# Kernel optimization log

Hardware: AMD Instinct MI355X
Metric: run time of the kernel (lower is better)

## Reference

```python
import jax, jax.numpy as jnp
import numpy as np

# Dimensions (see shape_source)
N = 50000       # graph_size (number of nodes)
E_HALF = 300000 # undirected edges
E = 2 * E_HALF  # directed edges (both orientations)
D = 4           # stalk dimension d
H = 32          # hidden_channels


def _build_graph(seed=0):
    """Symmetric directed edge list: columns [0,E_HALF) are (u->v), columns
    [E_HALF, E) are the reversed (v->u). opp_idx[e] is the index of the
    opposite orientation of edge e (this is exactly the pairing computed by
    lap.compute_left_right_map_index in the torch module)."""
    rng = np.random.default_rng(seed)
    u = rng.integers(0, N, size=E_HALF)
    v = rng.integers(0, N, size=E_HALF)
    v = np.where(v == u, (v + 1) % N, v)  # no self-loops
    edge_index = np.stack([np.concatenate([u, v]), np.concatenate([v, u])]).astype(np.int32)
    opp = np.concatenate([np.arange(E_HALF) + E_HALF, np.arange(E_HALF)]).astype(np.int32)
    return jnp.asarray(edge_index), jnp.asarray(opp)


def setup_inputs() -> dict:
    key = jax.random.key(0)
    k1, k2, k3 = jax.random.split(key, 3)
    edge_index, opp_idx = _build_graph()
    x = jax.random.normal(k1, (N, D, H), dtype=jnp.float32)
    Maps = jax.random.normal(k2, (E, D, D), dtype=jnp.float32)
    # linear1: torch.nn.Linear(d*d, prod(out_shape)) with out_shape=(d,d)
    W1 = jax.random.normal(k3, (D * D, D * D), dtype=jnp.float32) / np.sqrt(D * D)
    b1 = jnp.zeros((D * D,), dtype=jnp.float32)
    return {"x": x, "Maps": Maps, "W1": W1, "b1": b1,
            "edge_index": edge_index, "opp_idx": opp_idx}


def reference(x, Maps, W1, b1, edge_index, opp_idx):
    # The dual-graph (nodes = directed edges) sheaf Laplacian of the
    # GeneralLaplacianBuilder reduces to a closed per-edge block form:
    # every dual node has degree 1, so deg-normalisation (deg_normalised=True,
    # augmented=False) is the identity. For directed edge e = (s -> t) with
    # opposite edge e' = opp_idx[e]:
    #   diag block of dual node e           =  X_s X_s^T
    #   off-diag block between e and e'     = -X_s X_t^T
    # spmm(L, Maps^T-blocks) followed by the x2 and transpose in forward gives
    #   sims_e = 2 * ( M_e (X_s X_s^T) - M_{e'} (X_t X_s^T) )
    s, t = edge_index[0], edge_index[1]
    Xs = x[s]                                   # (E, D, H) gather
    Xt = x[t]                                   # (E, D, H) gather
    G_ss = jnp.einsum('edh,ekh->edk', Xs, Xs)   # (E, D, D)  X_s X_s^T
    G_ts = jnp.einsum('edh,ekh->edk', Xt, Xs)   # (E, D, D)  X_t X_s^T
    sims = 2.0 * (jnp.einsum('eij,ejk->eik', Maps, G_ss)
                  - jnp.einsum('eij,ejk->eik', Maps[opp_idx], G_ts))
    # linear1 (torch Linear: y = x W^T + b) + tanh activation
    flat = sims.reshape(E, D * D) @ W1.T + b1
    return jnp.tanh(flat).reshape(E, D, D)      # out_shape = (d, d)
```

## Files before the change

kernel.cpp:

```cpp
#include <hip/hip_runtime.h>

constexpr int TPB = 256;

__device__ __forceinline__ float fast_tanh(float v) {
    float ex = __expf(2.0f * v);
    return 1.0f - 2.0f * __builtin_amdgcn_rcpf(ex + 1.0f);
}

template <int CTRL>
__device__ __forceinline__ float dppadd(float x) {
    return x + __int_as_float(__builtin_amdgcn_update_dpp(
        0, __float_as_int(x), CTRL, 0xf, 0xf, true));
}
template <int CTRL>
__device__ __forceinline__ float dppmax(float x) {
    return fmaxf(x, __int_as_float(__builtin_amdgcn_update_dpp(
        0, __float_as_int(x), CTRL, 0xf, 0xf, true)));
}

__device__ __forceinline__ float rowsum16(float x) {
    x = dppadd<0x128>(x);
    x = dppadd<0x124>(x);
    x = dppadd<0x122>(x);
    x = dppadd<0x121>(x);
    return x;
}
__device__ __forceinline__ float rowmax16(float x) {
    x = dppmax<0x128>(x);
    x = dppmax<0x124>(x);
    x = dppmax<0x122>(x);
    x = dppmax<0x121>(x);
    return x;
}

__device__ __forceinline__ float2 unpack_q(unsigned int w) {
    return make_float2((float)((int)(w << 16) >> 16), (float)((int)w >> 16));
}

__global__ __launch_bounds__(TPB) void pack_q16_kernel(
    const float* __restrict__ x, uint4* __restrict__ xq,
    float* __restrict__ xscale, int N)
{
    const int tid  = blockIdx.x * TPB + threadIdx.x;
    const int node = tid >> 4, l = tid & 15;
    if (node >= N) return;
    const float* xr = x + (size_t)node * 128 + 2 * l;
    float2 f[4]; float m = 0.f;
    #pragma unroll
    for (int d = 0; d < 4; ++d) {
        f[d] = *(const float2*)(xr + d * 32);
        m = fmaxf(m, fmaxf(fabsf(f[d].x), fabsf(f[d].y)));
    }
    m = rowmax16(m);
    const float inv = m > 0.f ? 32767.0f / m : 0.f;
    unsigned int w[4];
    #pragma unroll
    for (int d = 0; d < 4; ++d) {
        int ix = (int)rintf(f[d].x * inv);
        int iy = (int)rintf(f[d].y * inv);
        w[d] = ((unsigned int)ix & 0xFFFFu) | ((unsigned int)iy << 16);
    }
    xq[(size_t)node * 16 + l] = make_uint4(w[0], w[1], w[2], w[3]);
    if (l == 0) xscale[node] = m * (1.0f / 32767.0f);
}

__global__ __launch_bounds__(TPB) void sheaf_q16_kernel(
    const uint4* __restrict__ xq,
    const float* __restrict__ xscale,
    const float* __restrict__ Maps,
    const float* __restrict__ W1,
    const float* __restrict__ b1,
    const int*   __restrict__ edge_index,
    const int*   __restrict__ opp_idx,
    float*       __restrict__ out,
    int E, int EHALF)
{
    const int tid  = threadIdx.x;
    const int l    = tid & 15;
    const int pair = (blockIdx.x * TPB + tid) >> 4;
    if (pair >= EHALF) return;

    const int s  = edge_index[pair];
    const int t  = edge_index[E + pair];
    const int e2 = opp_idx[pair];

    const uint4 qu = xq[(size_t)s * 16 + l];
    const uint4 qv = xq[(size_t)t * 16 + l];
    const float su = xscale[s];
    const float sv = xscale[t];

    float2 u[4], v[4];
    u[0] = unpack_q(qu.x); u[1] = unpack_q(qu.y);
    u[2] = unpack_q(qu.z); u[3] = unpack_q(qu.w);
    v[0] = unpack_q(qv.x); v[1] = unpack_q(qv.y);
    v[2] = unpack_q(qv.z); v[3] = unpack_q(qv.w);

    const float4* M1p = (const float4*)(Maps + (size_t)pair * 16);
    const float4* M2p = (const float4*)(Maps + (size_t)e2   * 16);
    float4 m1[4], m2[4];
    #pragma unroll
    for (int i = 0; i < 4; ++i) {
        float4 a = M1p[i], b = M2p[i];
        m1[i] = make_float4(a.x * su, a.y * su, a.z * su, a.w * su);
        m2[i] = make_float4(b.x * sv, b.y * sv, b.z * sv, b.w * sv);
    }

    float wr[16];
    {
        const float4* Wp = (const float4*)(W1 + l * 16);
        #pragma unroll
        for (int q4 = 0; q4 < 4; ++q4) {
            float4 w = Wp[q4];
            wr[q4*4+0] = w.x; wr[q4*4+1] = w.y; wr[q4*4+2] = w.z; wr[q4*4+3] = w.w;
        }
    }
    const float bias = b1[l];

    float2 Z[4];
    #pragma unroll
    for (int i = 0; i < 4; ++i) {
        float zx = m1[i].x * u[0].x;
        zx = fmaf(m1[i].y, u[1].x, zx);
        zx = fmaf(m1[i].z, u[2].x, zx);
        zx = fmaf(m1[i].w, u[3].x, zx);
        zx = fmaf(-m2[i].x, v[0].x, zx);
        zx = fmaf(-m2[i].y, v[1].x, zx);
        zx = fmaf(-m2[i].z, v[2].x, zx);
        zx = fmaf(-m2[i].w, v[3].x, zx);
        float zy = m1[i].x * u[0].y;
        zy = fmaf(m1[i].y, u[1].y, zy);
        zy = fmaf(m1[i].z, u[2].y, zy);
        zy = fmaf(m1[i].w, u[3].y, zy);
        zy = fmaf(-m2[i].x, v[0].y, zy);
        zy = fmaf(-m2[i].y, v[1].y, zy);
        zy = fmaf(-m2[i].z, v[2].y, zy);
        zy = fmaf(-m2[i].w, v[3].y, zy);
        Z[i] = make_float2(zx, zy);
    }

    float d1 = 0.f, d2 = 0.f;
    #pragma unroll
    for (int i = 0; i < 4; ++i) {
        #pragma unroll
        for (int k = 0; k < 4; ++k) {
            float pa = Z[i].x * u[k].x;
            pa = fmaf(Z[i].y, u[k].y, pa);
            float pb = Z[i].x * v[k].x;
            pb = fmaf(Z[i].y, v[k].y, pb);
            const float r1 = rowsum16(pa);
            const float r2 = rowsum16(pb);
            const int q = i * 4 + k;
            d1 = fmaf(wr[q], r1, d1);
            d2 = fmaf(wr[q], r2, d2);
        }
    }
    const float a1 = fmaf( 2.0f * su, d1, bias);
    const float a2 = fmaf(-2.0f * sv, d2, bias);

    out[(size_t)pair * 16 + l] = fast_tanh(a1);
    out[(size_t)e2   * 16 + l] = fast_tanh(a2);
}

__global__ __launch_bounds__(TPB) void sheaf_f32_kernel(
    const float* __restrict__ x, const float* __restrict__ Maps,
    const float* __restrict__ W1, const float* __restrict__ b1,
    const int* __restrict__ edge_index, const int* __restrict__ opp_idx,
    float* __restrict__ out, int E, int EHALF)
{
    const int tid  = threadIdx.x;
    const int l    = tid & 15;
    const int pair = (blockIdx.x * TPB + tid) >> 4;
    if (pair >= EHALF) return;
    const int s  = edge_index[pair];
    const int t  = edge_index[E + pair];
    const int e2 = opp_idx[pair];

    const float* xu = x + (size_t)s * 128 + 2 * l;
    const float* xv = x + (size_t)t * 128 + 2 * l;
    float2 u[4], v[4];
    #pragma unroll
    for (int d = 0; d < 4; ++d) {
        u[d] = *(const float2*)(xu + d * 32);
        v[d] = *(const float2*)(xv + d * 32);
    }
    const float4* M1p = (const float4*)(Maps + (size_t)pair * 16);
    const float4* M2p = (const float4*)(Maps + (size_t)e2   * 16);
    float4 m1[4], m2[4];
    #pragma unroll
    for (int i = 0; i < 4; ++i) { m1[i] = M1p[i]; m2[i] = M2p[i]; }
    float wr[16];
    {
        const float4* Wp = (const float4*)(W1 + l * 16);
        #pragma unroll
        for (int q4 = 0; q4 < 4; ++q4) {
            float4 w = Wp[q4];
            wr[q4*4+0] = w.x; wr[q4*4+1] = w.y; wr[q4*4+2] = w.z; wr[q4*4+3] = w.w;
        }
    }
    const float bias = b1[l];
    float2 Z[4];
    #pragma unroll
    for (int i = 0; i < 4; ++i) {
        float zx = m1[i].x * u[0].x;
        zx = fmaf(m1[i].y, u[1].x, zx);
        zx = fmaf(m1[i].z, u[2].x, zx);
        zx = fmaf(m1[i].w, u[3].x, zx);
        zx = fmaf(-m2[i].x, v[0].x, zx);
        zx = fmaf(-m2[i].y, v[1].x, zx);
        zx = fmaf(-m2[i].z, v[2].x, zx);
        zx = fmaf(-m2[i].w, v[3].x, zx);
        float zy = m1[i].x * u[0].y;
        zy = fmaf(m1[i].y, u[1].y, zy);
        zy = fmaf(m1[i].z, u[2].y, zy);
        zy = fmaf(m1[i].w, u[3].y, zy);
        zy = fmaf(-m2[i].x, v[0].y, zy);
        zy = fmaf(-m2[i].y, v[1].y, zy);
        zy = fmaf(-m2[i].z, v[2].y, zy);
        zy = fmaf(-m2[i].w, v[3].y, zy);
        Z[i] = make_float2(zx, zy);
    }
    float d1 = 0.f, d2 = 0.f;
    #pragma unroll
    for (int i = 0; i < 4; ++i) {
        #pragma unroll
        for (int k = 0; k < 4; ++k) {
            float pa = Z[i].x * u[k].x;
            pa = fmaf(Z[i].y, u[k].y, pa);
            float pb = Z[i].x * v[k].x;
            pb = fmaf(Z[i].y, v[k].y, pb);
            const float r1 = rowsum16(pa);
            const float r2 = rowsum16(pb);
            const int q = i * 4 + k;
            d1 = fmaf(wr[q], r1, d1);
            d2 = fmaf(wr[q], r2, d2);
        }
    }
    const float a1 = fmaf( 2.0f, d1, bias);
    const float a2 = fmaf(-2.0f, d2, bias);
    out[(size_t)pair * 16 + l] = fast_tanh(a1);
    out[(size_t)e2   * 16 + l] = fast_tanh(a2);
}

extern "C" void kernel_launch(void* const* d_in, const int* in_sizes, int n_in,
                              void* d_out, int out_size, void* d_ws, size_t ws_size,
                              hipStream_t stream) {
    const float* x          = (const float*)d_in[0];
    const float* Maps       = (const float*)d_in[1];
    const float* W1         = (const float*)d_in[2];
    const float* b1         = (const float*)d_in[3];
    const int*   edge_index = (const int*)d_in[4];
    const int*   opp_idx    = (const int*)d_in[5];

    const int N     = in_sizes[0] / 128;
    const int E     = in_sizes[5];
    const int EHALF = E / 2;

    const size_t q_bytes  = (size_t)N * 16 * sizeof(uint4);
    const size_t ws_need  = q_bytes + (size_t)N * sizeof(float);
    const int pair_blocks = (EHALF + 15) / 16;

    if (ws_size >= ws_need) {
        uint4* xq     = (uint4*)d_ws;
        float* xscale = (float*)((char*)d_ws + q_bytes);
        const int pack_blocks = (N * 16 + TPB - 1) / TPB;
        pack_q16_kernel<<<pack_blocks, TPB, 0, stream>>>(x, xq, xscale, N);
        sheaf_q16_kernel<<<pair_blocks, TPB, 0, stream>>>(
            xq, xscale, Maps, W1, b1, edge_index, opp_idx, (float*)d_out, E, EHALF);
    } else {
        sheaf_f32_kernel<<<pair_blocks, TPB, 0, stream>>>(
            x, Maps, W1, b1, edge_index, opp_idx, (float*)d_out, E, EHALF);
    }
}
```

Measured before the change: 59.82 us.

## Process each edge pair with 8 lanes instead of 16 using wider per-lane work

The quantized sheaf kernel now assigns 8 lanes per undirected edge pair (two pairs per 16-lane row), so each lane handles 4 hidden channels and 2 output entries. The cross-lane reductions drop from 4 DPP steps to 3, and the block count halves because each block covers 32 pairs. In exchange each lane loads more data and holds more registers, and the Maps loads move inside the i-loop, which may lower occupancy or memory-level parallelism.

```diff
diff --git a/kernel.cpp b/kernel.cpp
--- a/kernel.cpp
+++ b/kernel.cpp
@@ -1,6 +1,7 @@
 #include <hip/hip_runtime.h>
 
 constexpr int TPB = 256;
+constexpr int PAIRS_PER_BLOCK = 32;
 
 __device__ __forceinline__ float fast_tanh(float v) {
     float ex = __expf(2.0f * v);
@@ -19,17 +20,20 @@
 }
 
 __device__ __forceinline__ float rowsum16(float x) {
+    x = dppadd<0x128>(x); x = dppadd<0x124>(x);
+    x = dppadd<0x122>(x); x = dppadd<0x121>(x);
+    return x;
+}
+__device__ __forceinline__ float rowmax16(float x) {
+    x = dppmax<0x128>(x); x = dppmax<0x124>(x);
+    x = dppmax<0x122>(x); x = dppmax<0x121>(x);
+    return x;
+}
+
+__device__ __forceinline__ float sum8(float x) {
     x = dppadd<0x128>(x);
-    x = dppadd<0x124>(x);
-    x = dppadd<0x122>(x);
-    x = dppadd<0x121>(x);
-    return x;
-}
-__device__ __forceinline__ float rowmax16(float x) {
-    x = dppmax<0x128>(x);
-    x = dppmax<0x124>(x);
-    x = dppmax<0x122>(x);
-    x = dppmax<0x121>(x);
+    x = dppadd<0x39>(x);
+    x = dppadd<0x4E>(x);
     return x;
 }
 
@@ -64,7 +68,7 @@
     if (l == 0) xscale[node] = m * (1.0f / 32767.0f);
 }
 
-__global__ __launch_bounds__(TPB) void sheaf_q16_kernel(
+__global__ __launch_bounds__(TPB) void sheaf_q8_kernel(
     const uint4* __restrict__ xq,
     const float* __restrict__ xscale,
     const float* __restrict__ Maps,
@@ -75,36 +79,136 @@
     float*       __restrict__ out,
     int E, int EHALF)
 {
+    const int tid    = threadIdx.x;
+    const int lane16 = tid & 15;
+    const int row16  = tid >> 4;
+    const int pinr   = (lane16 >> 2) & 1;
+    const int slot   = (lane16 & 3) | (((lane16 >> 3) & 1) << 2);
+    const int pair   = blockIdx.x * PAIRS_PER_BLOCK + row16 * 2 + pinr;
+    if (pair >= EHALF) return;
+
+    const int s  = edge_index[pair];
+    const int t  = edge_index[E + pair];
+    const int e2 = opp_idx[pair];
+
+    const uint4* pu = xq + (size_t)s * 16 + 2 * slot;
+    const uint4* pv = xq + (size_t)t * 16 + 2 * slot;
+    const uint4 quA = pu[0], quB = pu[1];
+    const uint4 qvA = pv[0], qvB = pv[1];
+    const float su = xscale[s];
+    const float sv = xscale[t];
+
+    float4 u[4], v[4];
+    {
+        float2 a, b;
+        a = unpack_q(quA.x); b = unpack_q(quB.x); u[0] = make_float4(a.x, a.y, b.x, b.y);
+        a = unpack_q(quA.y); b = unpack_q(quB.y); u[1] = make_float4(a.x, a.y, b.x, b.y);
+        a = unpack_q(quA.z); b = unpack_q(quB.z); u[2] = make_float4(a.x, a.y, b.x, b.y);
+        a = unpack_q(quA.w); b = unpack_q(quB.w); u[3] = make_float4(a.x, a.y, b.x, b.y);
+        a = unpack_q(qvA.x); b = unpack_q(qvB.x); v[0] = make_float4(a.x, a.y, b.x, b.y);
+        a = unpack_q(qvA.y); b = unpack_q(qvB.y); v[1] = make_float4(a.x, a.y, b.x, b.y);
+        a = unpack_q(qvA.z); b = unpack_q(qvB.z); v[2] = make_float4(a.x, a.y, b.x, b.y);
+        a = unpack_q(qvA.w); b = unpack_q(qvB.w); v[3] = make_float4(a.x, a.y, b.x, b.y);
+    }
+
+    const int p0 = 2 * slot;
+    float wA[16], wB[16];
+    {
+        const float4* WpA = (const float4*)(W1 + p0 * 16);
+        const float4* WpB = (const float4*)(W1 + (p0 + 1) * 16);
+        #pragma unroll
+        for (int q4 = 0; q4 < 4; ++q4) {
+            float4 a = WpA[q4], b = WpB[q4];
+            wA[q4*4+0] = a.x; wA[q4*4+1] = a.y; wA[q4*4+2] = a.z; wA[q4*4+3] = a.w;
+            wB[q4*4+0] = b.x; wB[q4*4+1] = b.y; wB[q4*4+2] = b.z; wB[q4*4+3] = b.w;
+        }
+    }
+    const float2 bb = *(const float2*)(b1 + p0);
+
+    const float4* M1p = (const float4*)(Maps + (size_t)pair * 16);
+    const float4* M2p = (const float4*)(Maps + (size_t)e2   * 16);
+
+    float d1a = 0.f, d1b = 0.f, d2a = 0.f, d2b = 0.f;
+    #pragma unroll
+    for (int i = 0; i < 4; ++i) {
+        float4 m1 = M1p[i], m2 = M2p[i];
+        m1.x *= su; m1.y *= su; m1.z *= su; m1.w *= su;
+        m2.x *= sv; m2.y *= sv; m2.z *= sv; m2.w *= sv;
+
+        float4 zi;
+        zi.x = m1.x * u[0].x;            zi.y = m1.x * u[0].y;
+        zi.z = m1.x * u[0].z;            zi.w = m1.x * u[0].w;
+        zi.x = fmaf(m1.y, u[1].x, zi.x); zi.y = fmaf(m1.y, u[1].y, zi.y);
+        zi.z = fmaf(m1.y, u[1].z, zi.z); zi.w = fmaf(m1.y, u[1].w, zi.w);
+        zi.x = fmaf(m1.z, u[2].x, zi.x); zi.y = fmaf(m1.z, u[2].y, zi.y);
+        zi.z = fmaf(m1.z, u[2].z, zi.z); zi.w = fmaf(m1.z, u[2].w, zi.w);
+        zi.x = fmaf(m1.w, u[3].x, zi.x); zi.y = fmaf(m1.w, u[3].y, zi.y);
+        zi.z = fmaf(m1.w, u[3].z, zi.z); zi.w = fmaf(m1.w, u[3].w, zi.w);
+        zi.x = fmaf(-m2.x, v[0].x, zi.x); zi.y = fmaf(-m2.x, v[0].y, zi.y);
+        zi.z = fmaf(-m2.x, v[0].z, zi.z); zi.w = fmaf(-m2.x, v[0].w, zi.w);
+        zi.x = fmaf(-m2.y, v[1].x, zi.x); zi.y = fmaf(-m2.y, v[1].y, zi.y);
+        zi.z = fmaf(-m2.y, v[1].z, zi.z); zi.w = fmaf(-m2.y, v[1].w, zi.w);
+        zi.x = fmaf(-m2.z, v[2].x, zi.x); zi.y = fmaf(-m2.z, v[2].y, zi.y);
+        zi.z = fmaf(-m2.z, v[2].z, zi.z); zi.w = fmaf(-m2.z, v[2].w, zi.w);
+        zi.x = fmaf(-m2.w, v[3].x, zi.x); zi.y = fmaf(-m2.w, v[3].y, zi.y);
+        zi.z = fmaf(-m2.w, v[3].z, zi.z); zi.w = fmaf(-m2.w, v[3].w, zi.w);
+
+        #pragma unroll
+        for (int k = 0; k < 4; ++k) {
+            float pa = zi.x * u[k].x;
+            pa = fmaf(zi.y, u[k].y, pa);
+            pa = fmaf(zi.z, u[k].z, pa);
+            pa = fmaf(zi.w, u[k].w, pa);
+            float pb = zi.x * v[k].x;
+            pb = fmaf(zi.y, v[k].y, pb);
+            pb = fmaf(zi.z, v[k].z, pb);
+            pb = fmaf(zi.w, v[k].w, pb);
+            const float r1 = sum8(pa);
+            const float r2 = sum8(pb);
+            const int q = i * 4 + k;
+            d1a = fmaf(wA[q], r1, d1a);
+            d1b = fmaf(wB[q], r1, d1b);
+            d2a = fmaf(wA[q], r2, d2a);
+            d2b = fmaf(wB[q], r2, d2b);
+        }
+    }
+
+    const float o1a = fast_tanh(fmaf( 2.0f * su, d1a, bb.x));
+    const float o1b = fast_tanh(fmaf( 2.0f * su, d1b, bb.y));
+    const float o2a = fast_tanh(fmaf(-2.0f * sv, d2a, bb.x));
+    const float o2b = fast_tanh(fmaf(-2.0f * sv, d2b, bb.y));
+
+    *(float2*)(out + (size_t)pair * 16 + p0) = make_float2(o1a, o1b);
+    *(float2*)(out + (size_t)e2   * 16 + p0) = make_float2(o2a, o2b);
+}
+
+__global__ __launch_bounds__(TPB) void sheaf_f32_kernel(
+    const float* __restrict__ x, const float* __restrict__ Maps,
+    const float* __restrict__ W1, const float* __restrict__ b1,
+    const int* __restrict__ edge_index, const int* __restrict__ opp_idx,
+    float* __restrict__ out, int E, int EHALF)
+{
     const int tid  = threadIdx.x;
     const int l    = tid & 15;
     const int pair = (blockIdx.x * TPB + tid) >> 4;
     if (pair >= EHALF) return;
-
     const int s  = edge_index[pair];
     const int t  = edge_index[E + pair];
     const int e2 = opp_idx[pair];
 
-    const uint4 qu = xq[(size_t)s * 16 + l];
-    const uint4 qv = xq[(size_t)t * 16 + l];
-    const float su = xscale[s];
-    const float sv = xscale[t];
-
+    const float* xu = x + (size_t)s * 128 + 2 * l;
+    const float* xv = x + (size_t)t * 128 + 2 * l;
     float2 u[4], v[4];
-    u[0] = unpack_q(qu.x); u[1] = unpack_q(qu.y);
-    u[2] = unpack_q(qu.z); u[3] = unpack_q(qu.w);
-    v[0] = unpack_q(qv.x); v[1] = unpack_q(qv.y);
-    v[2] = unpack_q(qv.z); v[3] = unpack_q(qv.w);
-
+    #pragma unroll
+    for (int d = 0; d < 4; ++d) {
+        u[d] = *(const float2*)(xu + d * 32);
+        v[d] = *(const float2*)(xv + d * 32);
+    }
     const float4* M1p = (const float4*)(Maps + (size_t)pair * 16);
     const float4* M2p = (const float4*)(Maps + (size_t)e2   * 16);
     float4 m1[4], m2[4];
     #pragma unroll
-    for (int i = 0; i < 4; ++i) {
-        float4 a = M1p[i], b = M2p[i];
-        m1[i] = make_float4(a.x * su, a.y * su, a.z * su, a.w * su);
-        m2[i] = make_float4(b.x * sv, b.y * sv, b.z * sv, b.w * sv);
-    }
-
+    for (int i = 0; i < 4; ++i) { m1[i] = M1p[i]; m2[i] = M2p[i]; }
     float wr[16];
     {
         const float4* Wp = (const float4*)(W1 + l * 16);
@@ -115,7 +219,6 @@
         }
     }
     const float bias = b1[l];
-
     float2 Z[4];
     #pragma unroll
     for (int i = 0; i < 4; ++i) {
@@ -137,7 +240,6 @@
         zy = fmaf(-m2[i].w, v[3].y, zy);
         Z[i] = make_float2(zx, zy);
     }
-
     float d1 = 0.f, d2 = 0.f;
     #pragma unroll
     for (int i = 0; i < 4; ++i) {
@@ -154,87 +256,6 @@
             d2 = fmaf(wr[q], r2, d2);
         }
     }
-    const float a1 = fmaf( 2.0f * su, d1, bias);
-    const float a2 = fmaf(-2.0f * sv, d2, bias);
-
-    out[(size_t)pair * 16 + l] = fast_tanh(a1);
-    out[(size_t)e2   * 16 + l] = fast_tanh(a2);
-}
-
-__global__ __launch_bounds__(TPB) void sheaf_f32_kernel(
-    const float* __restrict__ x, const float* __restrict__ Maps,
-    const float* __restrict__ W1, const float* __restrict__ b1,
-    const int* __restrict__ edge_index, const int* __restrict__ opp_idx,
-    float* __restrict__ out, int E, int EHALF)
-{
-    const int tid  = threadIdx.x;
-    const int l    = tid & 15;
-    const int pair = (blockIdx.x * TPB + tid) >> 4;
-    if (pair >= EHALF) return;
-    const int s  = edge_index[pair];
-    const int t  = edge_index[E + pair];
-    const int e2 = opp_idx[pair];
-
-    const float* xu = x + (size_t)s * 128 + 2 * l;
-    const float* xv = x + (size_t)t * 128 + 2 * l;
-    float2 u[4], v[4];
-    #pragma unroll
-    for (int d = 0; d < 4; ++d) {
-        u[d] = *(const float2*)(xu + d * 32);
-        v[d] = *(const float2*)(xv + d * 32);
-    }
-    const float4* M1p = (const float4*)(Maps + (size_t)pair * 16);
-    const float4* M2p = (const float4*)(Maps + (size_t)e2   * 16);
-    float4 m1[4], m2[4];
-    #pragma unroll
-    for (int i = 0; i < 4; ++i) { m1[i] = M1p[i]; m2[i] = M2p[i]; }
-    float wr[16];
-    {
-        const float4* Wp = (const float4*)(W1 + l * 16);
-        #pragma unroll
-        for (int q4 = 0; q4 < 4; ++q4) {
-            float4 w = Wp[q4];
-            wr[q4*4+0] = w.x; wr[q4*4+1] = w.y; wr[q4*4+2] = w.z; wr[q4*4+3] = w.w;
-        }
-    }
-    const float bias = b1[l];
-    float2 Z[4];
-    #pragma unroll
-    for (int i = 0; i < 4; ++i) {
-        float zx = m1[i].x * u[0].x;
-        zx = fmaf(m1[i].y, u[1].x, zx);
-        zx = fmaf(m1[i].z, u[2].x, zx);
-        zx = fmaf(m1[i].w, u[3].x, zx);
-        zx = fmaf(-m2[i].x, v[0].x, zx);
-        zx = fmaf(-m2[i].y, v[1].x, zx);
-        zx = fmaf(-m2[i].z, v[2].x, zx);
-        zx = fmaf(-m2[i].w, v[3].x, zx);
-        float zy = m1[i].x * u[0].y;
-        zy = fmaf(m1[i].y, u[1].y, zy);
-        zy = fmaf(m1[i].z, u[2].y, zy);
-        zy = fmaf(m1[i].w, u[3].y, zy);
-        zy = fmaf(-m2[i].x, v[0].y, zy);
-        zy = fmaf(-m2[i].y, v[1].y, zy);
-        zy = fmaf(-m2[i].z, v[2].y, zy);
-        zy = fmaf(-m2[i].w, v[3].y, zy);
-        Z[i] = make_float2(zx, zy);
-    }
-    float d1 = 0.f, d2 = 0.f;
-    #pragma unroll
-    for (int i = 0; i < 4; ++i) {
-        #pragma unroll
-        for (int k = 0; k < 4; ++k) {
-            float pa = Z[i].x * u[k].x;
-            pa = fmaf(Z[i].y, u[k].y, pa);
-            float pb = Z[i].x * v[k].x;
-            pb = fmaf(Z[i].y, v[k].y, pb);
-            const float r1 = rowsum16(pa);
-            const float r2 = rowsum16(pb);
-            const int q = i * 4 + k;
-            d1 = fmaf(wr[q], r1, d1);
-            d2 = fmaf(wr[q], r2, d2);
-        }
-    }
     const float a1 = fmaf( 2.0f, d1, bias);
     const float a2 = fmaf(-2.0f, d2, bias);
     out[(size_t)pair * 16 + l] = fast_tanh(a1);
@@ -255,18 +276,19 @@
     const int E     = in_sizes[5];
     const int EHALF = E / 2;
 
-    const size_t q_bytes  = (size_t)N * 16 * sizeof(uint4);
-    const size_t ws_need  = q_bytes + (size_t)N * sizeof(float);
-    const int pair_blocks = (EHALF + 15) / 16;
+    const size_t q_bytes = (size_t)N * 16 * sizeof(uint4);
+    const size_t ws_need = q_bytes + (size_t)N * sizeof(float);
 
     if (ws_size >= ws_need) {
         uint4* xq     = (uint4*)d_ws;
         float* xscale = (float*)((char*)d_ws + q_bytes);
         const int pack_blocks = (N * 16 + TPB - 1) / TPB;
         pack_q16_kernel<<<pack_blocks, TPB, 0, stream>>>(x, xq, xscale, N);
-        sheaf_q16_kernel<<<pair_blocks, TPB, 0, stream>>>(
+        const int pair_blocks = (EHALF + PAIRS_PER_BLOCK - 1) / PAIRS_PER_BLOCK;
+        sheaf_q8_kernel<<<pair_blocks, TPB, 0, stream>>>(
             xq, xscale, Maps, W1, b1, edge_index, opp_idx, (float*)d_out, E, EHALF);
     } else {
+        const int pair_blocks = (EHALF + 15) / 16;
         sheaf_f32_kernel<<<pair_blocks, TPB, 0, stream>>>(
             x, Maps, W1, b1, edge_index, opp_idx, (float*)d_out, E, EHALF);
     }
```

Measured after the change: 69.89 us. 1.17x slower.
